# Kernel tuning notes

Hardware: AMD Instinct MI355X
Metric: run time of the kernel (lower is better)

Reference implementation:

```python
import jax, jax.numpy as jnp
import numpy as np

IN_FEATURES = 4096
OUT_FEATURES = 12288


def setup_inputs() -> dict:
    key = jax.random.key(0)
    k1, k2, k3 = jax.random.split(key, 3)
    inp = jax.random.normal(k1, (2, 2048, IN_FEATURES), dtype=jnp.float32)
    # int8 quantized weight, [out_features, in_features]
    quant_w = jax.random.randint(k2, (OUT_FEATURES, IN_FEATURES), -128, 128, dtype=jnp.int32).astype(jnp.int8)
    # per-output-channel scale, small positive (typical ~ max|w|/127)
    scale_w = (jax.random.uniform(k3, (OUT_FEATURES,), dtype=jnp.float32) + 0.5) * 0.02
    return {"inp": inp, "quant_w": quant_w, "scale_w": scale_w}


def reference(inp, quant_w, scale_w):
    # extract_weight_to_half: dequantize int8 weight with per-channel scale
    weight = quant_w.astype(inp.dtype) * scale_w[:, None]        # [N, K]
    # inp.view(-1, K) @ weight.T, reshaped back -> fuse via einsum
    out = jnp.einsum("bsk,nk->bsn", inp, weight)                 # [B, S, N]
    return out
```

## Files before the change

### kernel.cpp

```cpp
#include <hip/hip_runtime.h>
#include <hip/hip_bf16.h>


#define K_DIM 4096
#define N_DIM 12288

constexpr int BM = 256;
constexpr int BN = 256;
constexpr int BKB = 128;
constexpr int NT = K_DIM / BKB;

typedef float  f32x4  __attribute__((ext_vector_type(4)));
typedef int    i32x4  __attribute__((ext_vector_type(4)));
typedef short  bf16x8 __attribute__((ext_vector_type(8)));
typedef unsigned short u16x4 __attribute__((ext_vector_type(4)));

__device__ __forceinline__ unsigned short f32_to_bf16(float f) {
    unsigned int u = __builtin_bit_cast(unsigned int, f);
    u += 0x7FFFu + ((u >> 16) & 1u);
    return (unsigned short)(u >> 16);
}


__global__ __launch_bounds__(256)
void quant_a_kernel(const float* __restrict__ A,
                    signed char* __restrict__ Aq,
                    float* __restrict__ Ra) {
    const int row  = blockIdx.x;
    const int tid  = threadIdx.x;
    const int lane = tid & 63;
    const int wid  = tid >> 6;
    const float* arow = A + (size_t)row * K_DIM;
    const int base = tid * 16;

    f32x4 v[4];
    #pragma unroll
    for (int i = 0; i < 4; ++i)
        v[i] = *(const f32x4*)(arow + base + i * 4);

    float mx = 0.f;
    #pragma unroll
    for (int i = 0; i < 4; ++i)
        #pragma unroll
        for (int j = 0; j < 4; ++j)
            mx = fmaxf(mx, fabsf(v[i][j]));

    #pragma unroll
    for (int off = 32; off > 0; off >>= 1)
        mx = fmaxf(mx, __shfl_xor(mx, off));

    __shared__ float wmax[4];
    if (lane == 0) wmax[wid] = mx;
    __syncthreads();
    mx = fmaxf(fmaxf(wmax[0], wmax[1]), fmaxf(wmax[2], wmax[3]));

    const float inv = (mx > 0.f) ? (127.0f / mx) : 0.f;
    if (tid == 0) Ra[row] = mx * (1.0f / 127.0f);

    int p[4];
    #pragma unroll
    for (int i = 0; i < 4; ++i) {
        int b0 = (int)rintf(v[i][0] * inv);
        int b1 = (int)rintf(v[i][1] * inv);
        int b2 = (int)rintf(v[i][2] * inv);
        int b3 = (int)rintf(v[i][3] * inv);
        p[i] = (b0 & 255) | ((b1 & 255) << 8) | ((b2 & 255) << 16) | (b3 << 24);
    }
    *(i32x4*)(Aq + (size_t)row * K_DIM + base) = *(i32x4*)p;
}


__global__ __launch_bounds__(256)
void cvt_w8_kernel(const int* __restrict__ W, signed char* __restrict__ Wq, int n16) {
    int stride = gridDim.x * blockDim.x;
    for (int i = blockIdx.x * blockDim.x + threadIdx.x; i < n16; i += stride) {
        const int* src = W + (size_t)i * 16;
        int p[4];
        #pragma unroll
        for (int q = 0; q < 4; ++q) {
            const i32x4 w = *(const i32x4*)(src + q * 4);
            p[q] = (w[0] & 255) | ((w[1] & 255) << 8) | ((w[2] & 255) << 16) | (w[3] << 24);
        }
        *(i32x4*)(Wq + (size_t)i * 16) = *(i32x4*)p;
    }
}


__device__ __forceinline__ void gload_lds16(const void* g, void* l) {
    __builtin_amdgcn_global_load_lds(
        (const __attribute__((address_space(1))) unsigned int*)g,
        (__attribute__((address_space(3))) unsigned int*)l,
        16, 0, 0);
}

__global__ __launch_bounds__(512, 2)
void gemm_i8_256(const signed char* __restrict__ Aq,
                 const signed char* __restrict__ Wq,
                 const float* __restrict__ Sw,
                 const float* __restrict__ Ra,
                 float* __restrict__ Out,
                 int M) {
    __shared__ __align__(16) unsigned char As8[2][BM * BKB];
    __shared__ __align__(16) unsigned char Bs8[2][BN * BKB];

    const int tid  = threadIdx.x;
    const int lane = tid & 63;
    const int wid  = tid >> 6;
    const int wm   = wid >> 2;
    const int wn   = wid & 3;

    const int nwgy = M / BM;
    const int nwg  = (N_DIM / BN) * nwgy;
    const int cpx  = nwg >> 3;
    const int bid  = blockIdx.x;
    const int swz  = (bid & 7) * cpx + (bid >> 3);
    const int bx   = swz / nwgy;
    const int by   = swz % nwgy;
    const int bm   = by * BM;
    const int bn   = bx * BN;

    const int srow  = wid * 8 + (lane >> 3);
    const int scolB = ((lane & 7) ^ (lane >> 3)) * 16;

    #define STG_H(G, grow0, k0B, L)                                                 \
        do {                                                                        \
            gload_lds16((G) + (size_t)((grow0) + srow) * K_DIM + (k0B) + scolB,     \
                        (L) + wid * 1024);                                          \
            gload_lds16((G) + (size_t)((grow0) + 64 + srow) * K_DIM + (k0B) + scolB,\
                        (L) + 8192 + wid * 1024);                                   \
        } while (0)

    i32x4 acc[8][4];
    #pragma unroll
    for (int i = 0; i < 8; ++i)
        #pragma unroll
        for (int j = 0; j < 4; ++j)
            acc[i][j] = (i32x4){0, 0, 0, 0};

    const int c0   = lane & 15;
    const int kgB  = (lane >> 4) * 16;
    const int rswB = (c0 & 7) * 16;

    i32x4 af[8][2];
    i32x4 bf0[2][2];
    i32x4 bf1[2][2];

    const int aoffA = (wm * 128 + c0) * BKB;
    const int aoffB = (wn * 64 + c0) * BKB;

    #define RD_A(base, BUF, row0)                                                   \
        _Pragma("unroll") for (int mf = 0; mf < 4; ++mf)                            \
        _Pragma("unroll") for (int ks = 0; ks < 2; ++ks)                            \
            af[(base) + mf][ks] = *(const i32x4*)&As8[BUF][aoffA + ((row0) + mf * 16) * BKB + ((ks * 64 + kgB) ^ rswB)];

    #define RD_B(dst, BUF, row0)                                                    \
        _Pragma("unroll") for (int nf = 0; nf < 2; ++nf)                            \
        _Pragma("unroll") for (int ks = 0; ks < 2; ++ks)                            \
            (dst)[nf][ks] = *(const i32x4*)&Bs8[BUF][aoffB + ((row0) + nf * 16) * BKB + ((ks * 64 + kgB) ^ rswB)];

    #define CLUSTER(qm, qn, BF)                                                     \
        _Pragma("unroll") for (int ks = 0; ks < 2; ++ks)                            \
        _Pragma("unroll") for (int mf = 0; mf < 4; ++mf)                            \
        _Pragma("unroll") for (int nf = 0; nf < 2; ++nf)                            \
            acc[(qm)*4 + mf][(qn)*2 + nf] = __builtin_amdgcn_mfma_i32_16x16x64_i8(  \
                af[(qm)*4 + mf][ks], (BF)[nf][ks], acc[(qm)*4 + mf][(qn)*2 + nf],   \
                0, 0, 0);

    STG_H(Aq, bm,       0,   &As8[0][0]);
    STG_H(Aq, bm + 128, 0,   &As8[0][16384]);
    STG_H(Wq, bn,       0,   &Bs8[0][0]);
    STG_H(Wq, bn + 128, 0,   &Bs8[0][16384]);
    STG_H(Aq, bm,       BKB, &As8[1][0]);
    STG_H(Aq, bm + 128, BKB, &As8[1][16384]);
    asm volatile("s_waitcnt vmcnt(4)" ::: "memory");
    __builtin_amdgcn_s_barrier();

    for (int t = 0; t < NT; ++t) {
        const int cur = t & 1;
        unsigned char* Bnx  = &Bs8[cur ^ 1][0];
        unsigned char* Acur = &As8[cur][0];
        const int k1 = (t + 1) * BKB;
        const int k2 = (t + 2) * BKB;

        RD_A(0, cur, 0);
        RD_A(4, cur, 64);
        RD_B(bf0, cur, 0);
        if (t + 1 < NT) {
            STG_H(Wq, bn,       k1, Bnx);
            STG_H(Wq, bn + 128, k1, Bnx + 16384);
        }
        __builtin_amdgcn_s_barrier();
        asm volatile("s_waitcnt lgkmcnt(0)");
        __builtin_amdgcn_s_setprio(1);
        CLUSTER(0, 0, bf0);
        CLUSTER(1, 0, bf0);
        __builtin_amdgcn_s_setprio(0);
        __builtin_amdgcn_s_barrier();

        RD_B(bf1, cur, 32);
        if (t + 2 < NT) {
            STG_H(Aq, bm,       k2, Acur);
            STG_H(Aq, bm + 128, k2, Acur + 16384);
        }
        __builtin_amdgcn_s_barrier();
        asm volatile("s_waitcnt lgkmcnt(0)");
        __builtin_amdgcn_s_setprio(1);
        CLUSTER(0, 1, bf1);
        CLUSTER(1, 1, bf1);
        __builtin_amdgcn_s_setprio(0);
        if (t < NT - 2) {
            asm volatile("s_waitcnt vmcnt(4)" ::: "memory");
        } else if (t == NT - 2) {
            asm volatile("s_waitcnt vmcnt(0)" ::: "memory");
        }
        __builtin_amdgcn_s_barrier();
    }
    #undef CLUSTER
    #undef RD_A
    #undef RD_B
    #undef STG_H

    const int r0 = (lane >> 4) * 4;
    float rav[8][4];
    #pragma unroll
    for (int m = 0; m < 8; ++m)
        #pragma unroll
        for (int j = 0; j < 4; ++j)
            rav[m][j] = Ra[bm + wm * 128 + m * 16 + r0 + j];

    #pragma unroll
    for (int n = 0; n < 4; ++n) {
        const int col = bn + wn * 64 + n * 16 + c0;
        const float s = Sw[col];
        #pragma unroll
        for (int m = 0; m < 8; ++m) {
            const int rowb = bm + wm * 128 + m * 16 + r0;
            #pragma unroll
            for (int j = 0; j < 4; ++j)
                Out[(size_t)(rowb + j) * N_DIM + col] = (float)acc[m][n][j] * s * rav[m][j];
        }
    }
}


constexpr int FBM = 128, FBN = 128, FBK = 64, FPAD = 8;

__global__ __launch_bounds__(256)
void qlinear_fused_kernel(const float* __restrict__ A, const int* __restrict__ Wqi,
                          const float* __restrict__ Sw, float* __restrict__ Out, int M) {
    __shared__ unsigned short Asf[FBM][FBK + FPAD];
    __shared__ unsigned short Bsf[FBN][FBK + FPAD];
    const int tid  = threadIdx.x;
    const int lane = tid & 63;
    const int wid  = tid >> 6;
    const int wm   = wid >> 1;
    const int wn   = wid & 1;
    const int bm = blockIdx.y * FBM;
    const int bn = blockIdx.x * FBN;
    const int rowT = tid >> 4;
    const int kq   = tid & 15;
    f32x4 acc[4][4];
    #pragma unroll
    for (int i = 0; i < 4; ++i)
        #pragma unroll
        for (int j = 0; j < 4; ++j) acc[i][j] = (f32x4){0.f,0.f,0.f,0.f};
    const int c0 = lane & 15;
    const int kg = (lane >> 4) * 8;
    for (int k0 = 0; k0 < K_DIM; k0 += FBK) {
        #pragma unroll
        for (int it = 0; it < 8; ++it) {
            const int r = it * 16 + rowT;
            const f32x4 a4 = *(const f32x4*)(A + (size_t)(bm + r) * K_DIM + k0 + kq * 4);
            u16x4 h;
            h[0]=f32_to_bf16(a4[0]); h[1]=f32_to_bf16(a4[1]);
            h[2]=f32_to_bf16(a4[2]); h[3]=f32_to_bf16(a4[3]);
            *(u16x4*)&Asf[r][kq*4] = h;
        }
        #pragma unroll
        for (int it = 0; it < 8; ++it) {
            const int r = it * 16 + rowT;
            const i32x4 w4 = *(const i32x4*)(Wqi + (size_t)(bm + 0) * 0 + (size_t)(bn + r) * K_DIM + k0 + kq * 4);
            u16x4 h;
            h[0]=f32_to_bf16((float)w4[0]); h[1]=f32_to_bf16((float)w4[1]);
            h[2]=f32_to_bf16((float)w4[2]); h[3]=f32_to_bf16((float)w4[3]);
            *(u16x4*)&Bsf[r][kq*4] = h;
        }
        __syncthreads();
        #pragma unroll
        for (int ks = 0; ks < 2; ++ks) {
            const int kk = ks * 32 + kg;
            bf16x8 af2[4], bfr[4];
            #pragma unroll
            for (int mf = 0; mf < 4; ++mf)
                af2[mf] = *(const bf16x8*)&Asf[wm*64 + mf*16 + c0][kk];
            #pragma unroll
            for (int nf = 0; nf < 4; ++nf)
                bfr[nf] = *(const bf16x8*)&Bsf[wn*64 + nf*16 + c0][kk];
            #pragma unroll
            for (int mf = 0; mf < 4; ++mf)
                #pragma unroll
                for (int nf = 0; nf < 4; ++nf)
                    acc[mf][nf] = __builtin_amdgcn_mfma_f32_16x16x32_bf16(
                        af2[mf], bfr[nf], acc[mf][nf], 0, 0, 0);
        }
        __syncthreads();
    }
    const int r0 = (lane >> 4) * 4;
    #pragma unroll
    for (int nf = 0; nf < 4; ++nf) {
        const int col = bn + wn*64 + nf*16 + c0;
        const float s = Sw[col];
        #pragma unroll
        for (int mf = 0; mf < 4; ++mf) {
            const int rowb = bm + wm*64 + mf*16 + r0;
            #pragma unroll
            for (int j = 0; j < 4; ++j)
                Out[(size_t)(rowb + j) * N_DIM + col] = acc[mf][nf][j] * s;
        }
    }
}

extern "C" void kernel_launch(void* const* d_in, const int* in_sizes, int n_in,
                              void* d_out, int out_size, void* d_ws, size_t ws_size,
                              hipStream_t stream) {
    const float* inp = (const float*)d_in[0];
    const int*   qw  = (const int*)d_in[1];
    const float* sw  = (const float*)d_in[2];
    float*       out = (float*)d_out;

    const int M = in_sizes[0] / K_DIM;
    const size_t nA = (size_t)M * K_DIM;
    const size_t nW = (size_t)N_DIM * K_DIM;
    const size_t needQ = nA + nW + (size_t)M * sizeof(float);

    if (ws_size >= needQ && (M % BM) == 0) {
        signed char* Aq = (signed char*)d_ws;
        signed char* Wq8 = Aq + nA;
        float*       Ra = (float*)(Wq8 + nW);
        quant_a_kernel<<<M, 256, 0, stream>>>(inp, Aq, Ra);
        cvt_w8_kernel<<<2048, 256, 0, stream>>>(qw, Wq8, (int)(nW / 16));
        dim3 grid((N_DIM / BN) * (M / BM));
        gemm_i8_256<<<grid, 512, 0, stream>>>(Aq, Wq8, sw, Ra, out, M);
    } else {
        dim3 grid(N_DIM / FBN, M / FBM);
        qlinear_fused_kernel<<<grid, 256, 0, stream>>>(inp, qw, sw, out, M);
    }
}
```

Baseline: 314.1 us.

## Pack weights into MFMA fragment order and load B directly into registers

The weight conversion kernel now writes int8 weights in a layout where each 64-lane wave fragment is contiguous, so the GEMM can load B fragments straight from global memory into registers instead of staging them through LDS. This removes the B shared-memory buffers, halves LDS usage, and drops one barrier per iteration. A-tiles are still staged via LDS and the pipeline is reorganised around register prefetch of B for the next k-tile. The cost is more global traffic per wave (each wave reloads B rather than sharing through LDS) and longer global-load latency exposed to the MFMA loop.

```diff
diff --git a/kernel.cpp b/kernel.cpp
--- a/kernel.cpp
+++ b/kernel.cpp
@@ -71,17 +71,25 @@
 
 
 __global__ __launch_bounds__(256)
-void cvt_w8_kernel(const int* __restrict__ W, signed char* __restrict__ Wq, int n16) {
+void pack_w_kernel(const int* __restrict__ W, signed char* __restrict__ Wpk, int nchunk) {
     int stride = gridDim.x * blockDim.x;
-    for (int i = blockIdx.x * blockDim.x + threadIdx.x; i < n16; i += stride) {
-        const int* src = W + (size_t)i * 16;
+    for (int gid = blockIdx.x * blockDim.x + threadIdx.x; gid < nchunk; gid += stride) {
+        const int l   = gid & 63;
+        const int blk = gid >> 6;
+        const int ks  = blk & 1;
+        const int g   = (blk >> 1) & 15;
+        const int kt  = (blk >> 5) & 31;
+        const int B   = blk >> 10;
+        const int n   = B * 256 + (g >> 2) * 64 + (g & 3) * 16 + (l & 15);
+        const int kb  = kt * 128 + ks * 64 + ((l >> 4) * 16);
+        const int* src = W + (size_t)n * K_DIM + kb;
         int p[4];
         #pragma unroll
         for (int q = 0; q < 4; ++q) {
             const i32x4 w = *(const i32x4*)(src + q * 4);
             p[q] = (w[0] & 255) | ((w[1] & 255) << 8) | ((w[2] & 255) << 16) | (w[3] << 24);
         }
-        *(i32x4*)(Wq + (size_t)i * 16) = *(i32x4*)p;
+        *(i32x4*)(Wpk + (size_t)gid * 16) = *(i32x4*)p;
     }
 }
 
@@ -95,13 +103,12 @@
 
 __global__ __launch_bounds__(512, 2)
 void gemm_i8_256(const signed char* __restrict__ Aq,
-                 const signed char* __restrict__ Wq,
+                 const signed char* __restrict__ Wpk,
                  const float* __restrict__ Sw,
                  const float* __restrict__ Ra,
                  float* __restrict__ Out,
                  int M) {
     __shared__ __align__(16) unsigned char As8[2][BM * BKB];
-    __shared__ __align__(16) unsigned char Bs8[2][BN * BKB];
 
     const int tid  = threadIdx.x;
     const int lane = tid & 63;
@@ -122,12 +129,16 @@
     const int srow  = wid * 8 + (lane >> 3);
     const int scolB = ((lane & 7) ^ (lane >> 3)) * 16;
 
-    #define STG_H(G, grow0, k0B, L)                                                 \
-        do {                                                                        \
-            gload_lds16((G) + (size_t)((grow0) + srow) * K_DIM + (k0B) + scolB,     \
-                        (L) + wid * 1024);                                          \
-            gload_lds16((G) + (size_t)((grow0) + 64 + srow) * K_DIM + (k0B) + scolB,\
-                        (L) + 8192 + wid * 1024);                                   \
+    #define STG_A(k0B, L)                                                            \
+        do {                                                                         \
+            gload_lds16(Aq + (size_t)(bm + srow) * K_DIM + (k0B) + scolB,            \
+                        (L) + wid * 1024);                                           \
+            gload_lds16(Aq + (size_t)(bm + 64 + srow) * K_DIM + (k0B) + scolB,       \
+                        (L) + 8192 + wid * 1024);                                    \
+            gload_lds16(Aq + (size_t)(bm + 128 + srow) * K_DIM + (k0B) + scolB,      \
+                        (L) + 16384 + wid * 1024);                                   \
+            gload_lds16(Aq + (size_t)(bm + 192 + srow) * K_DIM + (k0B) + scolB,      \
+                        (L) + 24576 + wid * 1024);                                   \
         } while (0)
 
     i32x4 acc[8][4];
@@ -146,17 +157,19 @@
     i32x4 bf1[2][2];
 
     const int aoffA = (wm * 128 + c0) * BKB;
-    const int aoffB = (wn * 64 + c0) * BKB;
+
+    const signed char* Wbase = Wpk + ((size_t)((bn >> 8) * 32) << 10) * 32 + lane * 16;
+
+    #define LD_B(dst, kt, q0)                                                        \
+        _Pragma("unroll") for (int nf = 0; nf < 2; ++nf)                            \
+        _Pragma("unroll") for (int ks = 0; ks < 2; ++ks)                            \
+            (dst)[nf][ks] = *(const i32x4*)(Wbase +                                  \
+                ((size_t)((kt) * 32 + (wn * 4 + (q0) + nf) * 2 + (ks)) << 10));
 
     #define RD_A(base, BUF, row0)                                                   \
         _Pragma("unroll") for (int mf = 0; mf < 4; ++mf)                            \
         _Pragma("unroll") for (int ks = 0; ks < 2; ++ks)                            \
             af[(base) + mf][ks] = *(const i32x4*)&As8[BUF][aoffA + ((row0) + mf * 16) * BKB + ((ks * 64 + kgB) ^ rswB)];
-
-    #define RD_B(dst, BUF, row0)                                                    \
-        _Pragma("unroll") for (int nf = 0; nf < 2; ++nf)                            \
-        _Pragma("unroll") for (int ks = 0; ks < 2; ++ks)                            \
-            (dst)[nf][ks] = *(const i32x4*)&Bs8[BUF][aoffB + ((row0) + nf * 16) * BKB + ((ks * 64 + kgB) ^ rswB)];
 
     #define CLUSTER(qm, qn, BF)                                                     \
         _Pragma("unroll") for (int ks = 0; ks < 2; ++ks)                            \
@@ -166,59 +179,42 @@
                 af[(qm)*4 + mf][ks], (BF)[nf][ks], acc[(qm)*4 + mf][(qn)*2 + nf],   \
                 0, 0, 0);
 
-    STG_H(Aq, bm,       0,   &As8[0][0]);
-    STG_H(Aq, bm + 128, 0,   &As8[0][16384]);
-    STG_H(Wq, bn,       0,   &Bs8[0][0]);
-    STG_H(Wq, bn + 128, 0,   &Bs8[0][16384]);
-    STG_H(Aq, bm,       BKB, &As8[1][0]);
-    STG_H(Aq, bm + 128, BKB, &As8[1][16384]);
-    asm volatile("s_waitcnt vmcnt(4)" ::: "memory");
+    STG_A(0, &As8[0][0]);
+    LD_B(bf0, 0, 0);
+    STG_A(BKB, &As8[1][0]);
+    LD_B(bf1, 0, 2);
+    asm volatile("s_waitcnt vmcnt(8)" ::: "memory");
     __builtin_amdgcn_s_barrier();
 
     for (int t = 0; t < NT; ++t) {
         const int cur = t & 1;
-        unsigned char* Bnx  = &Bs8[cur ^ 1][0];
-        unsigned char* Acur = &As8[cur][0];
-        const int k1 = (t + 1) * BKB;
-        const int k2 = (t + 2) * BKB;
+        const int kt1 = (t + 1 < NT) ? (t + 1) : (NT - 1);
+        const int kt2 = (t + 2 < NT) ? (t + 2) : (NT - 1);
 
         RD_A(0, cur, 0);
         RD_A(4, cur, 64);
-        RD_B(bf0, cur, 0);
-        if (t + 1 < NT) {
-            STG_H(Wq, bn,       k1, Bnx);
-            STG_H(Wq, bn + 128, k1, Bnx + 16384);
-        }
         __builtin_amdgcn_s_barrier();
         asm volatile("s_waitcnt lgkmcnt(0)");
+        asm volatile("s_waitcnt vmcnt(8)" ::: "memory");
         __builtin_amdgcn_s_setprio(1);
         CLUSTER(0, 0, bf0);
         CLUSTER(1, 0, bf0);
         __builtin_amdgcn_s_setprio(0);
-        __builtin_amdgcn_s_barrier();
-
-        RD_B(bf1, cur, 32);
-        if (t + 2 < NT) {
-            STG_H(Aq, bm,       k2, Acur);
-            STG_H(Aq, bm + 128, k2, Acur + 16384);
-        }
-        __builtin_amdgcn_s_barrier();
-        asm volatile("s_waitcnt lgkmcnt(0)");
+
+        LD_B(bf0, kt1, 0);
+        STG_A(kt2 * BKB, &As8[cur][0]);
+        asm volatile("s_waitcnt vmcnt(8)" ::: "memory");
         __builtin_amdgcn_s_setprio(1);
         CLUSTER(0, 1, bf1);
         CLUSTER(1, 1, bf1);
         __builtin_amdgcn_s_setprio(0);
-        if (t < NT - 2) {
-            asm volatile("s_waitcnt vmcnt(4)" ::: "memory");
-        } else if (t == NT - 2) {
-            asm volatile("s_waitcnt vmcnt(0)" ::: "memory");
-        }
+        LD_B(bf1, kt1, 2);
         __builtin_amdgcn_s_barrier();
     }
     #undef CLUSTER
     #undef RD_A
-    #undef RD_B
-    #undef STG_H
+    #undef LD_B
+    #undef STG_A
 
     const int r0 = (lane >> 4) * 4;
     float rav[8][4];
@@ -279,7 +275,7 @@
         #pragma unroll
         for (int it = 0; it < 8; ++it) {
             const int r = it * 16 + rowT;
-            const i32x4 w4 = *(const i32x4*)(Wqi + (size_t)(bm + 0) * 0 + (size_t)(bn + r) * K_DIM + k0 + kq * 4);
+            const i32x4 w4 = *(const i32x4*)(Wqi + (size_t)(bn + r) * K_DIM + k0 + kq * 4);
             u16x4 h;
             h[0]=f32_to_bf16((float)w4[0]); h[1]=f32_to_bf16((float)w4[1]);
             h[2]=f32_to_bf16((float)w4[2]); h[3]=f32_to_bf16((float)w4[3]);
@@ -334,13 +330,13 @@
     const size_t needQ = nA + nW + (size_t)M * sizeof(float);
 
     if (ws_size >= needQ && (M % BM) == 0) {
-        signed char* Aq = (signed char*)d_ws;
-        signed char* Wq8 = Aq + nA;
-        float*       Ra = (float*)(Wq8 + nW);
+        signed char* Aq  = (signed char*)d_ws;
+        signed char* Wpk = Aq + nA;
+        float*       Ra  = (float*)(Wpk + nW);
         quant_a_kernel<<<M, 256, 0, stream>>>(inp, Aq, Ra);
-        cvt_w8_kernel<<<2048, 256, 0, stream>>>(qw, Wq8, (int)(nW / 16));
+        pack_w_kernel<<<2048, 256, 0, stream>>>(qw, Wpk, (int)(nW / 16));
         dim3 grid((N_DIM / BN) * (M / BM));
-        gemm_i8_256<<<grid, 512, 0, stream>>>(Aq, Wq8, sw, Ra, out, M);
+        gemm_i8_256<<<grid, 512, 0, stream>>>(Aq, Wpk, sw, Ra, out, M);
     } else {
         dim3 grid(N_DIM / FBN, M / FBM);
         qlinear_fused_kernel<<<grid, 256, 0, stream>>>(inp, qw, sw, out, M);
```

Result: no change. 319.6 us (+1.8%).
